# Kernel tuning notes

Hardware: AMD Instinct MI355X
Metric: run time of the kernel (lower is better)

## Reference

```python
import jax, jax.numpy as jnp
import numpy as np

D_MODEL = 128
N_HEADS = 4
HEAD_DIM = D_MODEL // N_HEADS


def setup_inputs() -> dict:
    key = jax.random.key(0)
    kx, kq, ko = jax.random.split(key, 3)
    B, T = 4, 4096
    x = jax.random.normal(kx, (B, T, D_MODEL), dtype=jnp.float32)
    s = 1.0 / np.sqrt(D_MODEL)
    # torch nn.Linear weight: [out, in]; y = x @ W.T
    W_qkv = jax.random.uniform(kq, (3 * D_MODEL, D_MODEL), dtype=jnp.float32, minval=-s, maxval=s)
    W_out = jax.random.uniform(ko, (D_MODEL, D_MODEL), dtype=jnp.float32, minval=-s, maxval=s)
    return {"x": x, "W_qkv": W_qkv, "W_out": W_out}


def reference(x, W_qkv, W_out):
    B, T, _ = x.shape
    qkv = (x @ W_qkv.T).reshape(B, T, 3, N_HEADS, HEAD_DIM)
    q, k, v = qkv[:, :, 0], qkv[:, :, 1], qkv[:, :, 2]  # [B,T,H,D]
    # scores: [B,H,T,T]
    scores = jnp.einsum('bthd,bshd->bhts', q, k) / jnp.sqrt(jnp.float32(HEAD_DIM))
    causal = jnp.triu(jnp.ones((T, T), dtype=bool), 1)
    scores = jnp.where(causal, -jnp.inf, scores)
    attn = jax.nn.softmax(scores, axis=-1)
    out = jnp.einsum('bhts,bshd->bthd', attn, v).reshape(B, T, D_MODEL)
    return out @ W_out.T
```

## Files before the change

kernel.cpp:

```cpp
#include <hip/hip_runtime.h>
#include <math.h>

#define B_   4
#define T_   4096
#define DM_  128
#define NH_  4
#define HD_  32
#define TOKENS (B_ * T_)

typedef __attribute__((ext_vector_type(8))) short short8;
typedef __attribute__((ext_vector_type(4))) float floatx4;

__device__ __forceinline__ unsigned short f2bf(float f) {
    union { float f; unsigned int u; } v; v.f = f;
    unsigned int u = v.u;
    u += 0x7fffu + ((u >> 16) & 1u);
    return (unsigned short)(u >> 16);
}
__device__ __forceinline__ void split_bf(float v, unsigned short& hi, unsigned short& lo) {
    unsigned short h = f2bf(v);
    float hf = __uint_as_float(((unsigned int)h) << 16);
    hi = h;
    lo = f2bf(v - hf);
}

#define LROW 136

__global__ __launch_bounds__(256) void qkv_proj_kernel(
    const float* __restrict__ x, const float* __restrict__ Wqkv,
    unsigned short* __restrict__ q_bf, unsigned short* __restrict__ k_bf,
    unsigned short* __restrict__ v_t)
{
    __shared__ __align__(16) unsigned short whi[64 * LROW];
    __shared__ __align__(16) unsigned short wlo[64 * LROW];

    const int tid  = threadIdx.x;
    const int wave = tid >> 6, lane = tid & 63;
    const int m    = lane & 15, q4 = lane >> 4;
    const int m0   = blockIdx.x * 64;
    const int ch   = blockIdx.y;
    const float scale = 0.2550052509571414f;

    {
        const float4* wg = (const float4*)(Wqkv + (size_t)ch * 64 * DM_);
        #pragma unroll
        for (int i = 0; i < 8; ++i) {
            const int f = tid + 256 * i;
            float4 v = wg[f];
            const int row = f >> 5, k4 = f & 31;
            ushort4 h, l;
            split_bf(v.x, h.x, l.x); split_bf(v.y, h.y, l.y);
            split_bf(v.z, h.z, l.z); split_bf(v.w, h.w, l.w);
            *(ushort4*)(whi + row * LROW + k4 * 4) = h;
            *(ushort4*)(wlo + row * LROW + k4 * 4) = l;
        }
    }

    short8 Ah[4], Al[4];
    {
        const float4* xg = (const float4*)(x + (size_t)(m0 + wave * 16 + m) * DM_);
        #pragma unroll
        for (int ks = 0; ks < 4; ++ks) {
            float4 a = xg[ks * 8 + q4 * 2];
            float4 b = xg[ks * 8 + q4 * 2 + 1];
            ushort4 h0, l0, h1, l1;
            split_bf(a.x, h0.x, l0.x); split_bf(a.y, h0.y, l0.y);
            split_bf(a.z, h0.z, l0.z); split_bf(a.w, h0.w, l0.w);
            split_bf(b.x, h1.x, l1.x); split_bf(b.y, h1.y, l1.y);
            split_bf(b.z, h1.z, l1.z); split_bf(b.w, h1.w, l1.w);
            Ah[ks] = short8{(short)h0.x, (short)h0.y, (short)h0.z, (short)h0.w,
                            (short)h1.x, (short)h1.y, (short)h1.z, (short)h1.w};
            Al[ks] = short8{(short)l0.x, (short)l0.y, (short)l0.z, (short)l0.w,
                            (short)l1.x, (short)l1.y, (short)l1.z, (short)l1.w};
        }
    }
    __syncthreads();

    floatx4 acc[4];
    #pragma unroll
    for (int nb = 0; nb < 4; ++nb) {
        floatx4 a = {0.f, 0.f, 0.f, 0.f};
        #pragma unroll
        for (int ks = 0; ks < 4; ++ks) {
            short8 Bh = *(const short8*)(whi + (nb * 16 + m) * LROW + ks * 32 + q4 * 8);
            short8 Bl = *(const short8*)(wlo + (nb * 16 + m) * LROW + ks * 32 + q4 * 8);
            a = __builtin_amdgcn_mfma_f32_16x16x32_bf16(Ah[ks], Bh, a, 0, 0, 0);
            a = __builtin_amdgcn_mfma_f32_16x16x32_bf16(Ah[ks], Bl, a, 0, 0, 0);
            a = __builtin_amdgcn_mfma_f32_16x16x32_bf16(Al[ks], Bh, a, 0, 0, 0);
        }
        acc[nb] = a;
    }
    __syncthreads();

    unsigned short* stage = whi;
    const bool isV = (ch >= 4);
    if (isV) {
        #pragma unroll
        for (int nb = 0; nb < 4; ++nb) {
            ushort4 p;
            p.x = f2bf(acc[nb][0]); p.y = f2bf(acc[nb][1]);
            p.z = f2bf(acc[nb][2]); p.w = f2bf(acc[nb][3]);
            *(ushort4*)(stage + (nb * 16 + m) * 72 + wave * 16 + q4 * 4) = p;
        }
    } else {
        const float scl = (ch < 2) ? scale : 1.0f;
        #pragma unroll
        for (int nb = 0; nb < 4; ++nb)
            #pragma unroll
            for (int reg = 0; reg < 4; ++reg)
                stage[(wave * 16 + q4 * 4 + reg) * 72 + nb * 16 + m]
                    = f2bf(acc[nb][reg] * scl);
    }
    __syncthreads();

    const int b    = m0 >> 12;
    const int t0   = m0 & (T_ - 1);
    const int head = tid >> 7;
    const int hh   = (ch * 2 + head) & 3;
    const int bh   = b * NH_ + hh;
    const int r    = tid & 127;
    if (isV) {
        const int d = r >> 2, qc = r & 3;
        const unsigned short* sp = stage + (head * 32 + d) * 72 + qc * 16;
        short8 v0 = *(const short8*)(sp);
        short8 v1 = *(const short8*)(sp + 8);
        unsigned short* gp = v_t + ((size_t)bh * HD_ + d) * T_ + t0 + qc * 16;
        *(short8*)(gp)     = v0;
        *(short8*)(gp + 8) = v1;
    } else {
        unsigned short* dst = (ch < 2) ? q_bf : k_bf;
        const int t = r >> 1, half = r & 1;
        const unsigned short* sp = stage + t * 72 + head * 32 + half * 16;
        short8 v0 = *(const short8*)(sp);
        short8 v1 = *(const short8*)(sp + 8);
        unsigned short* gp = dst + ((size_t)bh * T_ + t0 + t) * HD_ + half * 16;
        *(short8*)(gp)     = v0;
        *(short8*)(gp + 8) = v1;
    }
}

template<bool LAST>
__device__ __forceinline__ void attn_tile128(
    const char* kLds, const char* vLds, char* pT,
    const int m, const int q4, const short8 qf, const short8 ones,
    const int sbN_in, const int limit,
    floatx4& O0, floatx4& O1, float& mx, float& ls)
{
    const int sbN = LAST ? sbN_in : 8;
    const int kN  = sbN >> 1;

    floatx4 st[8];
    #pragma unroll
    for (int sb = 0; sb < 8; ++sb) {
        if (sb >= sbN) continue;
        short8 kfrag = *(const short8*)(kLds + (sb * 16 + m) * 80 + q4 * 16);
        floatx4 z = {0.f, 0.f, 0.f, 0.f};
        st[sb] = __builtin_amdgcn_mfma_f32_16x16x32_bf16(kfrag, qf, z, 0, 0, 0);
    }

    if (LAST) {
        #pragma unroll
        for (int sb = 0; sb < 8; ++sb) {
            if (sb >= sbN) continue;
            #pragma unroll
            for (int reg = 0; reg < 4; ++reg)
                if (sb * 16 + q4 * 4 + reg > limit) st[sb][reg] = -INFINITY;
        }
    }

    float fm[8];
    #pragma unroll
    for (int sb = 0; sb < 8; ++sb)
        fm[sb] = (sb < sbN) ? fmaxf(fmaxf(st[sb][0], st[sb][1]),
                                    fmaxf(st[sb][2], st[sb][3]))
                            : -INFINITY;
    float rmax = fmaxf(fmaxf(fmaxf(fm[0], fm[1]), fmaxf(fm[2], fm[3])),
                       fmaxf(fmaxf(fm[4], fm[5]), fmaxf(fm[6], fm[7])));
    rmax = fmaxf(rmax, __shfl_xor(rmax, 16, 64));
    rmax = fmaxf(rmax, __shfl_xor(rmax, 32, 64));

    const float mn = fmaxf(mx, rmax);
    const float alpha = __builtin_amdgcn_exp2f(mx - mn);
    mx = mn;

    #pragma unroll
    for (int sb = 0; sb < 8; ++sb) {
        if (sb >= sbN) continue;
        float p0 = __builtin_amdgcn_exp2f(st[sb][0] - mn);
        float p1 = __builtin_amdgcn_exp2f(st[sb][1] - mn);
        float p2 = __builtin_amdgcn_exp2f(st[sb][2] - mn);
        float p3 = __builtin_amdgcn_exp2f(st[sb][3] - mn);
        unsigned u0 = __float_as_uint(p0) + 0x8000u;
        unsigned u1 = __float_as_uint(p1) + 0x8000u;
        unsigned u2 = __float_as_uint(p2) + 0x8000u;
        unsigned u3 = __float_as_uint(p3) + 0x8000u;
        uint2 pk;
        pk.x = __builtin_amdgcn_perm(u1, u0, 0x07060302);
        pk.y = __builtin_amdgcn_perm(u3, u2, 0x07060302);
        *(uint2*)(pT + ((((2 * sb + (q4 >> 1)) ^ m) << 4) + (q4 & 1) * 8)) = pk;
    }
    #pragma unroll
    for (int reg = 0; reg < 4; ++reg) { O0[reg] *= alpha; O1[reg] *= alpha; }

    __asm__ volatile("s_waitcnt lgkmcnt(0)" ::: "memory");
    __builtin_amdgcn_sched_barrier(0);

    floatx4 ps = {0.f, 0.f, 0.f, 0.f};
    #pragma unroll
    for (int ks = 0; ks < 4; ++ks) {
        if (ks >= kN) continue;
        short8 bfrag = *(const short8*)(pT + (((ks * 4 + q4) ^ m) << 4));
        short8 va = *(const short8*)(vLds + m * 272 + ks * 64 + q4 * 16);
        short8 vb = *(const short8*)(vLds + (16 + m) * 272 + ks * 64 + q4 * 16);
        O0 = __builtin_amdgcn_mfma_f32_16x16x32_bf16(va, bfrag, O0, 0, 0, 0);
        O1 = __builtin_amdgcn_mfma_f32_16x16x32_bf16(vb, bfrag, O1, 0, 0, 0);
        ps = __builtin_amdgcn_mfma_f32_16x16x32_bf16(ones, bfrag, ps, 0, 0, 0);
    }
    ls = ls * alpha + ps[0];
}

__global__ __launch_bounds__(256, 4) void attn_mfma_kernel(
    const unsigned short* __restrict__ qb, const unsigned short* __restrict__ kb,
    const unsigned short* __restrict__ vtb, float* __restrict__ og)
{
    __shared__ __align__(16) char smem[10240 + 8704 + 4 * 4096];
    char* kLds = smem;
    char* vLds = smem + 10240;
    const int tid  = threadIdx.x;
    const int wave = tid >> 6, lane = tid & 63;
    const int m    = lane & 15, q4 = lane >> 4;
    char* pT = smem + 18944 + wave * 4096 + m * 256;

    const int pid = blockIdx.x;
    const int xcd = pid & 7;
    const int r_  = pid >> 3;
    const int bh  = xcd * 2 + (r_ & 1);
    const int j_  = r_ >> 1;
    const int a_  = j_ & 15, k_ = j_ >> 4;
    const int qt  = (k_ == 0) ? a_ : (k_ == 1) ? 63 - a_
                  : (k_ == 2) ? 32 + a_ : 31 - a_;

    const size_t qkbase = (size_t)bh * T_ * HD_;
    const char* kg = (const char*)(kb + qkbase);
    const char* vg = (const char*)(vtb + qkbase);

    short8 qf = *(const short8*)((const char*)(qb + qkbase)
                 + (size_t)(qt * 64 + wave * 16 + m) * 64 + q4 * 16);
    const int qrow = wave * 16 + m;

    const short8 ones = short8{(short)0x3F80, (short)0x3F80, (short)0x3F80,
                               (short)0x3F80, (short)0x3F80, (short)0x3F80,
                               (short)0x3F80, (short)0x3F80};

    floatx4 O0 = {0.f, 0.f, 0.f, 0.f}, O1 = {0.f, 0.f, 0.f, 0.f};
    float mx = -INFINITY, ls = 0.f;

    const int itN      = (qt >> 1) + 1;
    const int sbN_last = (qt & 1) ? 8 : 4;
    const int limit    = ((qt & 1) << 6) + qrow;

    const int krow = tid >> 2, ku = tid & 3;
    const int vd = tid >> 3, vu = tid & 7;
    const char* kstage = kg + (size_t)krow * 64 + ku * 16;
    const char* vstage = vg + (size_t)vd * (T_ * 2) + vu * 16;

    short8 sk0 = *(const short8*)(kstage);
    short8 sk1 = *(const short8*)(kstage + 64 * 64);
    short8 sv0 = *(const short8*)(vstage);
    short8 sv1 = *(const short8*)(vstage + 128);

    for (int it = 0; it < itN; ++it) {
        __syncthreads();
        *(short8*)(kLds + krow * 80 + ku * 16) = sk0;
        *(short8*)(kLds + (64 + krow) * 80 + ku * 16) = sk1;
        *(short8*)(vLds + vd * 272 + vu * 16) = sv0;
        *(short8*)(vLds + vd * 272 + 128 + vu * 16) = sv1;
        __syncthreads();

        if (it + 1 < itN) {
            const size_t nb = (size_t)(it + 1) << 7;
            sk0 = *(const short8*)(kstage + nb * 64);
            sk1 = *(const short8*)(kstage + nb * 64 + 64 * 64);
            sv0 = *(const short8*)(vstage + nb * 2);
            sv1 = *(const short8*)(vstage + nb * 2 + 128);
            attn_tile128<false>(kLds, vLds, pT, m, q4, qf, ones, 8, 0,
                                O0, O1, mx, ls);
        } else {
            attn_tile128<true>(kLds, vLds, pT, m, q4, qf, ones, sbN_last, limit,
                               O0, O1, mx, ls);
        }
    }

    const float inv = 1.f / ls;
    const int b = bh >> 2, h = bh & 3;
    const int t = qt * 64 + qrow;
    float* orow = og + (((size_t)b * T_ + t) * NH_ + h) * HD_;
    *(float4*)(orow + q4 * 4)      = make_float4(O0[0] * inv, O0[1] * inv,
                                                 O0[2] * inv, O0[3] * inv);
    *(float4*)(orow + 16 + q4 * 4) = make_float4(O1[0] * inv, O1[1] * inv,
                                                 O1[2] * inv, O1[3] * inv);
}

__global__ __launch_bounds__(256) void out_proj_kernel(
    const float* __restrict__ a, const float* __restrict__ Wout,
    float* __restrict__ out)
{
    __shared__ __align__(16) unsigned short whi[64 * LROW];
    __shared__ __align__(16) unsigned short wlo[64 * LROW];

    const int tid  = threadIdx.x;
    const int wave = tid >> 6, lane = tid & 63;
    const int m    = lane & 15, q4 = lane >> 4;
    const int m0   = blockIdx.x * 64;
    const int ch   = blockIdx.y;

    {
        const float4* wg = (const float4*)(Wout + (size_t)ch * 64 * DM_);
        #pragma unroll
        for (int i = 0; i < 8; ++i) {
            const int f = tid + 256 * i;
            float4 v = wg[f];
            const int row = f >> 5, k4 = f & 31;
            ushort4 h, l;
            split_bf(v.x, h.x, l.x); split_bf(v.y, h.y, l.y);
            split_bf(v.z, h.z, l.z); split_bf(v.w, h.w, l.w);
            *(ushort4*)(whi + row * LROW + k4 * 4) = h;
            *(ushort4*)(wlo + row * LROW + k4 * 4) = l;
        }
    }

    short8 Ah[4], Al[4];
    {
        const float4* xg = (const float4*)(a + (size_t)(m0 + wave * 16 + m) * DM_);
        #pragma unroll
        for (int ks = 0; ks < 4; ++ks) {
            float4 av = xg[ks * 8 + q4 * 2];
            float4 bv = xg[ks * 8 + q4 * 2 + 1];
            ushort4 h0, l0, h1, l1;
            split_bf(av.x, h0.x, l0.x); split_bf(av.y, h0.y, l0.y);
            split_bf(av.z, h0.z, l0.z); split_bf(av.w, h0.w, l0.w);
            split_bf(bv.x, h1.x, l1.x); split_bf(bv.y, h1.y, l1.y);
            split_bf(bv.z, h1.z, l1.z); split_bf(bv.w, h1.w, l1.w);
            Ah[ks] = short8{(short)h0.x, (short)h0.y, (short)h0.z, (short)h0.w,
                            (short)h1.x, (short)h1.y, (short)h1.z, (short)h1.w};
            Al[ks] = short8{(short)l0.x, (short)l0.y, (short)l0.z, (short)l0.w,
                            (short)l1.x, (short)l1.y, (short)l1.z, (short)l1.w};
        }
    }
    __syncthreads();

    #pragma unroll
    for (int nb = 0; nb < 4; ++nb) {
        floatx4 acc = {0.f, 0.f, 0.f, 0.f};
        #pragma unroll
        for (int ks = 0; ks < 4; ++ks) {
            short8 Bh = *(const short8*)(whi + (nb * 16 + m) * LROW + ks * 32 + q4 * 8);
            short8 Bl = *(const short8*)(wlo + (nb * 16 + m) * LROW + ks * 32 + q4 * 8);
            acc = __builtin_amdgcn_mfma_f32_16x16x32_bf16(Ah[ks], Bh, acc, 0, 0, 0);
            acc = __builtin_amdgcn_mfma_f32_16x16x32_bf16(Ah[ks], Bl, acc, 0, 0, 0);
            acc = __builtin_amdgcn_mfma_f32_16x16x32_bf16(Al[ks], Bh, acc, 0, 0, 0);
        }
        const int n = ch * 64 + nb * 16 + m;
        const int tok0 = m0 + wave * 16 + q4 * 4;
        #pragma unroll
        for (int reg = 0; reg < 4; ++reg)
            out[(size_t)(tok0 + reg) * DM_ + n] = acc[reg];
    }
}

extern "C" void kernel_launch(void* const* d_in, const int* in_sizes, int n_in,
                              void* d_out, int out_size, void* d_ws, size_t ws_size,
                              hipStream_t stream) {
    const float* x    = (const float*)d_in[0];
    const float* Wqkv = (const float*)d_in[1];
    const float* Wout = (const float*)d_in[2];
    float* out = (float*)d_out;

    char* ws = (char*)d_ws;
    unsigned short* q_bf  = (unsigned short*)(ws);
    unsigned short* k_bf  = (unsigned short*)(ws + (size_t)4 * 1024 * 1024);
    unsigned short* v_t   = (unsigned short*)(ws + (size_t)8 * 1024 * 1024);
    float*          att_ws = (float*)(ws + (size_t)12 * 1024 * 1024);

    qkv_proj_kernel<<<dim3(TOKENS / 64, 6), 256, 0, stream>>>(x, Wqkv, q_bf, k_bf, v_t);
    attn_mfma_kernel<<<1024, 256, 0, stream>>>(q_bf, k_bf, v_t, att_ws);
    out_proj_kernel<<<dim3(TOKENS / 64, 2), 256, 0, stream>>>(att_ws, Wout, out);
}
```

Before: 129.4 us.

## Fuse output projection into attention kernel via per-head atomic accumulation

Removes the separate out_proj kernel and the fp32 attention workspace round trip. Each attention block writes its normalized head output to LDS, loads and splits its head's 32-column slice of W_out into bf16 hi/lo, and multiplies with MFMA. It then atomically adds the partial products into the output, which is zeroed by a memset first. This trades one kernel launch and a 8MB write/read for four-way fp32 atomic contention per output element, redundant W_out loading per block, and a memset.

Measured after the change: 137.5 us. +6.2%, slower.

```diff
diff --git a/kernel.cpp b/kernel.cpp
--- a/kernel.cpp
+++ b/kernel.cpp
@@ -221,7 +221,8 @@
 
 __global__ __launch_bounds__(256, 4) void attn_mfma_kernel(
     const unsigned short* __restrict__ qb, const unsigned short* __restrict__ kb,
-    const unsigned short* __restrict__ vtb, float* __restrict__ og)
+    const unsigned short* __restrict__ vtb, const float* __restrict__ Wout,
+    float* __restrict__ out)
 {
     __shared__ __align__(16) char smem[10240 + 8704 + 4 * 4096];
     char* kLds = smem;
@@ -291,80 +292,64 @@
         }
     }
 
-    const float inv = 1.f / ls;
-    const int b = bh >> 2, h = bh & 3;
-    const int t = qt * 64 + qrow;
-    float* orow = og + (((size_t)b * T_ + t) * NH_ + h) * HD_;
-    *(float4*)(orow + q4 * 4)      = make_float4(O0[0] * inv, O0[1] * inv,
-                                                 O0[2] * inv, O0[3] * inv);
-    *(float4*)(orow + 16 + q4 * 4) = make_float4(O1[0] * inv, O1[1] * inv,
-                                                 O1[2] * inv, O1[3] * inv);
-}
-
-__global__ __launch_bounds__(256) void out_proj_kernel(
-    const float* __restrict__ a, const float* __restrict__ Wout,
-    float* __restrict__ out)
-{
-    __shared__ __align__(16) unsigned short whi[64 * LROW];
-    __shared__ __align__(16) unsigned short wlo[64 * LROW];
-
-    const int tid  = threadIdx.x;
-    const int wave = tid >> 6, lane = tid & 63;
-    const int m    = lane & 15, q4 = lane >> 4;
-    const int m0   = blockIdx.x * 64;
-    const int ch   = blockIdx.y;
-
-    {
-        const float4* wg = (const float4*)(Wout + (size_t)ch * 64 * DM_);
-        #pragma unroll
-        for (int i = 0; i < 8; ++i) {
+    __syncthreads();
+    float*          oLds = (float*)smem;
+    unsigned short* wHi  = (unsigned short*)(smem + 10240);
+    unsigned short* wLo  = (unsigned short*)(smem + 18944);
+
+    const int h = bh & 3, b = bh >> 2;
+    {
+        const float inv = 1.f / ls;
+        float* orow = oLds + qrow * 36;
+        *(float4*)(orow + q4 * 4)      = make_float4(O0[0] * inv, O0[1] * inv,
+                                                     O0[2] * inv, O0[3] * inv);
+        *(float4*)(orow + 16 + q4 * 4) = make_float4(O1[0] * inv, O1[1] * inv,
+                                                     O1[2] * inv, O1[3] * inv);
+    }
+    {
+        #pragma unroll
+        for (int i = 0; i < 16; ++i) {
             const int f = tid + 256 * i;
-            float4 v = wg[f];
-            const int row = f >> 5, k4 = f & 31;
-            ushort4 h, l;
-            split_bf(v.x, h.x, l.x); split_bf(v.y, h.y, l.y);
-            split_bf(v.z, h.z, l.z); split_bf(v.w, h.w, l.w);
-            *(ushort4*)(whi + row * LROW + k4 * 4) = h;
-            *(ushort4*)(wlo + row * LROW + k4 * 4) = l;
-        }
-    }
-
-    short8 Ah[4], Al[4];
-    {
-        const float4* xg = (const float4*)(a + (size_t)(m0 + wave * 16 + m) * DM_);
-        #pragma unroll
-        for (int ks = 0; ks < 4; ++ks) {
-            float4 av = xg[ks * 8 + q4 * 2];
-            float4 bv = xg[ks * 8 + q4 * 2 + 1];
-            ushort4 h0, l0, h1, l1;
-            split_bf(av.x, h0.x, l0.x); split_bf(av.y, h0.y, l0.y);
-            split_bf(av.z, h0.z, l0.z); split_bf(av.w, h0.w, l0.w);
-            split_bf(bv.x, h1.x, l1.x); split_bf(bv.y, h1.y, l1.y);
-            split_bf(bv.z, h1.z, l1.z); split_bf(bv.w, h1.w, l1.w);
-            Ah[ks] = short8{(short)h0.x, (short)h0.y, (short)h0.z, (short)h0.w,
-                            (short)h1.x, (short)h1.y, (short)h1.z, (short)h1.w};
-            Al[ks] = short8{(short)l0.x, (short)l0.y, (short)l0.z, (short)l0.w,
-                            (short)l1.x, (short)l1.y, (short)l1.z, (short)l1.w};
-        }
-    }
-    __syncthreads();
-
-    #pragma unroll
-    for (int nb = 0; nb < 4; ++nb) {
+            const int n = f >> 5, k = f & 31;
+            float w = Wout[n * DM_ + h * 32 + k];
+            unsigned short hi_, lo_;
+            split_bf(w, hi_, lo_);
+            wHi[n * 34 + k] = hi_;
+            wLo[n * 34 + k] = lo_;
+        }
+    }
+    __syncthreads();
+
+    short8 Ah_, Al_;
+    {
+        const float* ap = oLds + (wave * 16 + m) * 36 + q4 * 8;
+        float4 a0 = *(const float4*)(ap);
+        float4 a1 = *(const float4*)(ap + 4);
+        ushort4 h0, l0, h1, l1;
+        split_bf(a0.x, h0.x, l0.x); split_bf(a0.y, h0.y, l0.y);
+        split_bf(a0.z, h0.z, l0.z); split_bf(a0.w, h0.w, l0.w);
+        split_bf(a1.x, h1.x, l1.x); split_bf(a1.y, h1.y, l1.y);
+        split_bf(a1.z, h1.z, l1.z); split_bf(a1.w, h1.w, l1.w);
+        Ah_ = short8{(short)h0.x, (short)h0.y, (short)h0.z, (short)h0.w,
+                     (short)h1.x, (short)h1.y, (short)h1.z, (short)h1.w};
+        Al_ = short8{(short)l0.x, (short)l0.y, (short)l0.z, (short)l0.w,
+                     (short)l1.x, (short)l1.y, (short)l1.z, (short)l1.w};
+    }
+
+    #pragma unroll
+    for (int nb = 0; nb < 8; ++nb) {
+        short8 Bh = *(const short8*)(wHi + (nb * 16 + m) * 34 + q4 * 8);
+        short8 Bl = *(const short8*)(wLo + (nb * 16 + m) * 34 + q4 * 8);
         floatx4 acc = {0.f, 0.f, 0.f, 0.f};
-        #pragma unroll
-        for (int ks = 0; ks < 4; ++ks) {
-            short8 Bh = *(const short8*)(whi + (nb * 16 + m) * LROW + ks * 32 + q4 * 8);
-            short8 Bl = *(const short8*)(wlo + (nb * 16 + m) * LROW + ks * 32 + q4 * 8);
-            acc = __builtin_amdgcn_mfma_f32_16x16x32_bf16(Ah[ks], Bh, acc, 0, 0, 0);
-            acc = __builtin_amdgcn_mfma_f32_16x16x32_bf16(Ah[ks], Bl, acc, 0, 0, 0);
-            acc = __builtin_amdgcn_mfma_f32_16x16x32_bf16(Al[ks], Bh, acc, 0, 0, 0);
-        }
-        const int n = ch * 64 + nb * 16 + m;
-        const int tok0 = m0 + wave * 16 + q4 * 4;
-        #pragma unroll
-        for (int reg = 0; reg < 4; ++reg)
-            out[(size_t)(tok0 + reg) * DM_ + n] = acc[reg];
+        acc = __builtin_amdgcn_mfma_f32_16x16x32_bf16(Ah_, Bh, acc, 0, 0, 0);
+        acc = __builtin_amdgcn_mfma_f32_16x16x32_bf16(Ah_, Bl, acc, 0, 0, 0);
+        acc = __builtin_amdgcn_mfma_f32_16x16x32_bf16(Al_, Bh, acc, 0, 0, 0);
+        const int n = nb * 16 + m;
+        #pragma unroll
+        for (int reg = 0; reg < 4; ++reg) {
+            const int t = qt * 64 + wave * 16 + q4 * 4 + reg;
+            atomicAdd(out + ((size_t)b * T_ + t) * DM_ + n, acc[reg]);
+        }
     }
 }
 
@@ -380,9 +365,9 @@
     unsigned short* q_bf  = (unsigned short*)(ws);
     unsigned short* k_bf  = (unsigned short*)(ws + (size_t)4 * 1024 * 1024);
     unsigned short* v_t   = (unsigned short*)(ws + (size_t)8 * 1024 * 1024);
-    float*          att_ws = (float*)(ws + (size_t)12 * 1024 * 1024);
+
+    hipMemsetAsync(out, 0, (size_t)TOKENS * DM_ * sizeof(float), stream);
 
     qkv_proj_kernel<<<dim3(TOKENS / 64, 6), 256, 0, stream>>>(x, Wqkv, q_bf, k_bf, v_t);
-    attn_mfma_kernel<<<1024, 256, 0, stream>>>(q_bf, k_bf, v_t, att_ws);
-    out_proj_kernel<<<dim3(TOKENS / 64, 2), 256, 0, stream>>>(att_ws, Wout, out);
-}
+    attn_mfma_kernel<<<1024, 256, 0, stream>>>(q_bf, k_bf, v_t, Wout, out);
+}
```
